# Kernel optimization log

Measured on AMD Instinct MI355X. Metric: run time of the kernel, lower is better.

Reference implementation:

```python
import jax, jax.numpy as jnp
import numpy as np

B, T, I, F, M, O = 256, 512, 128, 512, 512, 128


def setup_inputs() -> dict:
    key = jax.random.key(0)
    ks = jax.random.split(key, 12)
    def lin(k, out_d, in_d):
        std = 1.0 / np.sqrt(in_d)
        kw, kb = jax.random.split(k)
        W = jax.random.uniform(kw, (out_d, in_d), jnp.float32, -std, std)
        b = jax.random.uniform(kb, (out_d,), jnp.float32, -std, std)
        return W, b
    Wi2f, bi2f = lin(ks[0], F, I)
    Wm2f, bm2f = lin(ks[1], F, M)
    Wf2m, bf2m = lin(ks[2], M, F)
    Wm2m, bm2m = lin(ks[3], M, M)
    Wout, bout = lin(ks[4], O, M)
    x = jax.random.normal(ks[5], (B, T, I), jnp.float32)
    m0 = jnp.zeros((B, M), jnp.float32)
    return {"x": x, "m0": m0,
            "Wi2f": Wi2f, "bi2f": bi2f, "Wm2f": Wm2f, "bm2f": bm2f,
            "Wf2m": Wf2m, "bf2m": bf2m, "Wm2m": Wm2m, "bm2m": bm2m,
            "Wout": Wout, "bout": bout}


def reference(x, m0, Wi2f, bi2f, Wm2f, bm2f, Wf2m, bf2m, Wm2m, bm2m, Wout, bout):
    # Precompute input->functional projection for all timesteps (batched GEMM).
    xp = jnp.einsum('bti,fi->btf', x, Wi2f) + bi2f  # (B, T, F)

    def step(m, xp_t):
        f = jnp.tanh(xp_t + m @ Wm2f.T + bm2f)           # (B, F)
        m_new = (f @ Wf2m.T + bf2m) + (m @ Wm2m.T + bm2m)  # (B, M)
        return m_new, m_new

    m_last, _ms = jax.lax.scan(step, m0, jnp.swapaxes(xp, 0, 1))  # ms: (T, B, M)
    # OUTPUT_TYPE.LAST_OUT: output layer applied to final memory state.
    return m_last @ Wout.T + bout  # (B, O)
```

## Files before the change

### kernel.cpp

```cpp
#include <hip/hip_runtime.h>
#include <hip/hip_bf16.h>

typedef __bf16 bf16x8 __attribute__((ext_vector_type(8)));
typedef __bf16 bf16x4 __attribute__((ext_vector_type(4)));
typedef float  f32x4  __attribute__((ext_vector_type(4)));
typedef unsigned int u32;
typedef unsigned long long u64;

static __device__ __forceinline__ void mfma_z(f32x4& d, bf16x8 a, const f32x4& b) {
    asm("v_mfma_f32_16x16x32_bf16 %0, %1, %2, 0"
        : "=&v"(d) : "v"(a), "a"(b));
}
static __device__ __forceinline__ void mfma_a(f32x4& d, bf16x8 a, const f32x4& b) {
    asm("v_mfma_f32_16x16x32_bf16 %0, %1, %2, %0"
        : "+v"(d) : "v"(a), "a"(b));
}
#define ACC_GUARD(e, o) asm volatile("s_nop 7\n\ts_nop 7" : "+v"(e), "+v"(o))

static __device__ __forceinline__ f32x4 mfma16(bf16x8 a, bf16x8 b, f32x4 c) {
    return __builtin_amdgcn_mfma_f32_16x16x32_bf16(a, b, c, 0, 0, 0);
}

static __device__ __forceinline__ void poll_flags(const u32* flags, u32 tgt,
                                                  int lane, u32& alive) {
    if (!alive) return;
    for (u32 it = 0; it < (1u << 20); ++it) {
        u32 v = __hip_atomic_load(&flags[lane & 7], __ATOMIC_RELAXED, __HIP_MEMORY_SCOPE_AGENT);
        if (__all((int)(v >= tgt))) return;
        __builtin_amdgcn_s_sleep(1);
    }
    alive = 0;
}

#define TLEN 512
#define IDIM 128
#define FDIM 512
#define MDIM 512
#define ODIM 128
#define BC   16
#define NGRP 16
#define NCU  8
#define PSTR 520
#define XSTR 136

#define WS_WI   0
#define WS_W2F  (WS_WI  + FDIM*IDIM*2)
#define WS_W2M  (WS_W2F + FDIM*MDIM*2)
#define WS_WF2  (WS_W2M + MDIM*MDIM*2)
#define WS_WO   (WS_WF2 + MDIM*FDIM*2)
#define WS_C    (WS_WO  + ODIM*MDIM*2)
#define WS_D    (WS_C   + FDIM*FDIM*2)
#define WS_B1   (WS_D   + MDIM*FDIM*2)
#define WS_B23  (WS_B1  + FDIM*4)
#define WS_CB   (WS_B23 + MDIM*4)
#define WS_CU   (WS_CB  + FDIM*4)
#define WS_FLG  (WS_CU  + MDIM*4)
#define WS_BUF  (WS_FLG + NGRP*64*4)

#define N_WI  (FDIM*IDIM)
#define N_W2F (FDIM*MDIM)
#define N_W2M (MDIM*MDIM)
#define N_WF2 (MDIM*FDIM)
#define N_WO  (ODIM*MDIM)

__global__ __launch_bounds__(256) void lmn_prep1(
    const float* __restrict__ Wi2f, const float* __restrict__ Wm2f,
    const float* __restrict__ Wm2m, const float* __restrict__ Wf2m,
    const float* __restrict__ Wout,
    const float* __restrict__ bi2f, const float* __restrict__ bm2f,
    const float* __restrict__ bf2m, const float* __restrict__ bm2m,
    __bf16* __restrict__ WI, __bf16* __restrict__ W2F, __bf16* __restrict__ W2M,
    __bf16* __restrict__ WF2, __bf16* __restrict__ WO,
    float* __restrict__ b1, float* __restrict__ b23, u32* __restrict__ flags)
{
    int i = blockIdx.x * 256 + threadIdx.x;
    if (i < N_WI)  { WI[i]  = (__bf16)Wi2f[i]; return; }  i -= N_WI;
    if (i < N_W2F) { W2F[i] = (__bf16)Wm2f[i]; return; }  i -= N_W2F;
    if (i < N_W2M) { W2M[i] = (__bf16)Wm2m[i]; return; }  i -= N_W2M;
    if (i < N_WF2) { WF2[i] = (__bf16)Wf2m[i]; return; }  i -= N_WF2;
    if (i < N_WO)  { WO[i]  = (__bf16)Wout[i]; return; }  i -= N_WO;
    if (i < FDIM)  { b1[i]  = bi2f[i] + bm2f[i]; return; } i -= FDIM;
    if (i < MDIM)  { b23[i] = bf2m[i] + bm2m[i]; return; } i -= MDIM;
    if (i < NGRP * 64) { flags[i] = 0u; return; }
}

__global__ __launch_bounds__(256) void lmn_prep2(
    const float* __restrict__ Wm2f, const float* __restrict__ Wm2m,
    const float* __restrict__ Wf2m,
    const float* __restrict__ b1, const float* __restrict__ b23,
    __bf16* __restrict__ C, __bf16* __restrict__ D,
    float* __restrict__ cb, float* __restrict__ cu)
{
    int bb = blockIdx.x;
    if (bb < 2048) {
        int row = bb >> 1;
        int k   = (bb & 1) * 256 + threadIdx.x;
        const float* A = (row < 512) ? Wm2f : Wm2m;
        int r = row & 511;
        float acc = 0.f;
        for (int j = 0; j < 512; ++j)
            acc += A[(size_t)r * 512 + j] * Wf2m[(size_t)j * 512 + k];
        if (row < 512) C[(size_t)r * 512 + k] = (__bf16)acc;
        else           D[(size_t)r * 512 + k] = (__bf16)acc;
        return;
    }
    int idx = (bb - 2048) * 256 + threadIdx.x;
    if (idx < 512) {
        float acc = b1[idx];
        for (int j = 0; j < 512; ++j) acc += Wm2f[(size_t)idx * 512 + j] * b23[j];
        cb[idx] = acc;
    } else {
        int r = idx - 512;
        float acc = 0.f;
        for (int j = 0; j < 512; ++j) acc += Wm2m[(size_t)r * 512 + j] * b23[j];
        cu[r] = acc;
    }
}

__global__ __launch_bounds__(512, 2) void lmn_scan(
    const float* __restrict__ x, const float* __restrict__ m0,
    const __bf16* __restrict__ WI, const __bf16* __restrict__ W2F,
    const __bf16* __restrict__ W2M, const __bf16* __restrict__ Cm,
    const __bf16* __restrict__ Dm, const __bf16* __restrict__ WF2,
    const __bf16* __restrict__ WO,
    const float* __restrict__ b1, const float* __restrict__ cb,
    const float* __restrict__ cu, const float* __restrict__ b23,
    const float* __restrict__ bout,
    u32* __restrict__ flags_all, __bf16* __restrict__ buf,
    float* __restrict__ out)
{
    __shared__ __bf16 ulds[BC][PSTR];
    __shared__ __bf16 flds[BC][PSTR];
    __shared__ __bf16 xlds[BC][XSTR];

    const int tid  = threadIdx.x;
    const int lane = tid & 63;
    const int w    = tid >> 6;
    const int wq   = w & 3;
    const int l15  = lane & 15;
    const int l4   = lane >> 4;
    const int koff = 8 * l4;
    const bool sRole = (w < 4);

    const int b = blockIdx.x;
    const int g = b & 15;
    const int p = b >> 4;
    const int row0 = g * BC;

    u32* flags = flags_all + g * 64;
    u32  alive = 1;

    const int c0 = 64 * p + 16 * wq + l15;

    f32x4 wgt[36];
    {
        const __bf16* rA = (sRole ? W2F : W2M) + (size_t)c0 * MDIM;
        const __bf16* rC = (sRole ? Cm  : Dm ) + (size_t)c0 * FDIM;
        #pragma unroll
        for (int j = 0; j < 16; ++j) {
            wgt[j]      = *(const f32x4*)&rA[j * 32 + koff];
            wgt[16 + j] = *(const f32x4*)&rC[j * 32 + koff];
        }
        if (sRole) {
            const __bf16* rX = WI + (size_t)c0 * IDIM;
            #pragma unroll
            for (int j = 0; j < 4; ++j) wgt[32 + j] = *(const f32x4*)&rX[j * 32 + koff];
        } else {
            #pragma unroll
            for (int j = 32; j < 36; ++j) wgt[j] = f32x4{0, 0, 0, 0};
        }
        #pragma unroll
        for (int j = 0; j < 36; ++j) asm volatile("" : "+a"(wgt[j]));
    }
    const float b1r = sRole ? b1[c0] : 0.f;
    const float cbr = sRole ? cb[c0] : 0.f;
    const float cur = sRole ? 0.f    : cu[c0];

    #pragma unroll
    for (int i = 0; i < 2; ++i) {
        int c = tid + 512 * i;
        int row = c >> 6, col8 = (c & 63) << 3;
        const float* ms = &m0[(size_t)(row0 + row) * MDIM + col8];
        float4 v0 = ((const float4*)ms)[0], v1 = ((const float4*)ms)[1];
        *(bf16x8*)&ulds[row][col8] =
            bf16x8{(__bf16)v0.x, (__bf16)v0.y, (__bf16)v0.z, (__bf16)v0.w,
                   (__bf16)v1.x, (__bf16)v1.y, (__bf16)v1.z, (__bf16)v1.w};
    }
    if (tid < 256) {
        int rr = tid >> 4, c8 = (tid & 15) << 3;
        const float* xs = &x[(size_t)(row0 + rr) * TLEN * IDIM + c8];
        float4 v0 = ((const float4*)xs)[0], v1 = ((const float4*)xs)[1];
        *(bf16x8*)&xlds[rr][c8] =
            bf16x8{(__bf16)v0.x, (__bf16)v0.y, (__bf16)v0.z, (__bf16)v0.w,
                   (__bf16)v1.x, (__bf16)v1.y, (__bf16)v1.z, (__bf16)v1.w};
    }
    __syncthreads();

    f32x4 accE, accO;
    {
        bf16x8 a0 = *(const bf16x8*)&ulds[l15][0 * 32 + koff];
        bf16x8 a1 = *(const bf16x8*)&ulds[l15][1 * 32 + koff];
        mfma_z(accE, a0, wgt[0]);  mfma_z(accO, a1, wgt[1]);
        #pragma unroll
        for (int j = 2; j < 16; ++j) {
            bf16x8 am = *(const bf16x8*)&ulds[l15][j * 32 + koff];
            if (j & 1) mfma_a(accO, am, wgt[j]);
            else       mfma_a(accE, am, wgt[j]);
        }
        if (sRole) {
            #pragma unroll
            for (int j = 0; j < 4; ++j) {
                bf16x8 ax = *(const bf16x8*)&xlds[l15][j * 32 + koff];
                if (j & 1) mfma_a(accO, ax, wgt[32 + j]);
                else       mfma_a(accE, ax, wgt[32 + j]);
            }
        }
    }

    for (int t = 0; t < TLEN; ++t) {
        __syncthreads();

        ACC_GUARD(accE, accO);
        f32x4 va = accE + accO;
        if (sRole) {
            const float addc = (t == 0) ? b1r : cbr;
            #pragma unroll
            for (int r = 0; r < 4; ++r)
                flds[4 * l4 + r][c0] = (__bf16)tanhf(va[r] + addc);
        } else {
            const float addu = (t == 0) ? 0.f : cur;
            #pragma unroll
            for (int r = 0; r < 4; ++r)
                ulds[4 * l4 + r][c0] = (__bf16)(va[r] + addu);
        }
        __syncthreads();

        const size_t bufbase = (size_t)((t & 1) * NGRP + g) * (2 * BC * MDIM);
        {
            int mat = tid >> 8;
            int rr = (tid & 255) >> 4, c4 = (tid & 15) << 2;
            const __bf16* src = mat ? &flds[rr][64 * p + c4] : &ulds[rr][64 * p + c4];
            u64 v = *(const u64*)src;
            __hip_atomic_store((u64*)(buf + bufbase + (size_t)mat * (BC * MDIM)
                                      + rr * MDIM + 64 * p + c4),
                               v, __ATOMIC_RELAXED, __HIP_MEMORY_SCOPE_AGENT);
        }
        asm volatile("s_waitcnt vmcnt(0)" ::: "memory");
        __syncthreads();
        if (tid == 0)
            __hip_atomic_store(&flags[p], (u32)t + 1u,
                               __ATOMIC_RELAXED, __HIP_MEMORY_SCOPE_AGENT);

        if (tid < 256 && t + 1 < TLEN) {
            int rr = tid >> 4, c8 = (tid & 15) << 3;
            const float* xs = &x[((size_t)(row0 + rr) * TLEN + (t + 1)) * IDIM + c8];
            float4 v0 = ((const float4*)xs)[0], v1 = ((const float4*)xs)[1];
            *(bf16x8*)&xlds[rr][c8] =
                bf16x8{(__bf16)v0.x, (__bf16)v0.y, (__bf16)v0.z, (__bf16)v0.w,
                       (__bf16)v1.x, (__bf16)v1.y, (__bf16)v1.z, (__bf16)v1.w};
        }
        poll_flags(flags, (u32)t + 1u, lane, alive);

        #pragma unroll
        for (int i = 0; i < 4; ++i) {
            int c = tid + 512 * i;
            int mat = c >> 10, rem = c & 1023;
            int row = rem >> 6, col8 = (rem & 63) << 3;
            const __bf16* src = buf + bufbase + (size_t)mat * (BC * MDIM)
                              + row * MDIM + col8;
            u64 lo = __hip_atomic_load((const u64*)src,     __ATOMIC_RELAXED, __HIP_MEMORY_SCOPE_AGENT);
            u64 hi = __hip_atomic_load((const u64*)src + 1, __ATOMIC_RELAXED, __HIP_MEMORY_SCOPE_AGENT);
            union { u64 q[2]; bf16x8 v; } uu; uu.q[0] = lo; uu.q[1] = hi;
            if (mat) *(bf16x8*)&flds[row][col8] = uu.v;
            else     *(bf16x8*)&ulds[row][col8] = uu.v;
        }
        __syncthreads();

        if (t == TLEN - 1) break;

        {
            bf16x8 a0 = *(const bf16x8*)&ulds[l15][0 * 32 + koff];
            bf16x8 a1 = *(const bf16x8*)&ulds[l15][1 * 32 + koff];
            mfma_z(accE, a0, wgt[0]);  mfma_z(accO, a1, wgt[1]);
            #pragma unroll
            for (int j = 2; j < 16; ++j) {
                bf16x8 am = *(const bf16x8*)&ulds[l15][j * 32 + koff];
                if (j & 1) mfma_a(accO, am, wgt[j]);
                else       mfma_a(accE, am, wgt[j]);
            }
            #pragma unroll
            for (int j = 0; j < 16; ++j) {
                bf16x8 af = *(const bf16x8*)&flds[l15][j * 32 + koff];
                if (j & 1) mfma_a(accO, af, wgt[16 + j]);
                else       mfma_a(accE, af, wgt[16 + j]);
            }
            if (sRole) {
                #pragma unroll
                for (int j = 0; j < 4; ++j) {
                    bf16x8 ax = *(const bf16x8*)&xlds[l15][j * 32 + koff];
                    if (j & 1) mfma_a(accO, ax, wgt[32 + j]);
                    else       mfma_a(accE, ax, wgt[32 + j]);
                }
            }
        }
    }

    if (p == 0) {
        f32x4 ma[4];
        #pragma unroll
        for (int nt = 0; nt < 4; ++nt) {
            int ct = 64 * w + 16 * nt + l15;
            f32x4 acc = {0, 0, 0, 0};
            #pragma unroll
            for (int j = 0; j < 16; ++j) {
                bf16x8 af = *(const bf16x8*)&flds[l15][j * 32 + koff];
                bf16x8 bw = *(const bf16x8*)&WF2[(size_t)ct * FDIM + j * 32 + koff];
                acc = mfma16(af, bw, acc);
            }
            ma[nt] = acc;
        }
        #pragma unroll
        for (int nt = 0; nt < 4; ++nt) {
            int ct = 64 * w + 16 * nt + l15;
            #pragma unroll
            for (int r = 0; r < 4; ++r) {
                float mv = ma[nt][r] + (float)ulds[4 * l4 + r][ct] + b23[ct];
                ulds[4 * l4 + r][ct] = (__bf16)mv;
            }
        }
        __syncthreads();
        const int oc = 16 * w + l15;
        const __bf16* ro = WO + (size_t)oc * MDIM;
        f32x4 oe = {0, 0, 0, 0}, oo = {0, 0, 0, 0};
        #pragma unroll
        for (int j = 0; j < 16; ++j) {
            bf16x8 am = *(const bf16x8*)&ulds[l15][j * 32 + koff];
            bf16x8 bw = *(const bf16x8*)&ro[j * 32 + koff];
            if (j & 1) oo = mfma16(am, bw, oo); else oe = mfma16(am, bw, oe);
        }
        f32x4 oa = oe + oo;
        const float bo = bout[oc];
        #pragma unroll
        for (int r = 0; r < 4; ++r)
            out[(size_t)(row0 + 4 * l4 + r) * ODIM + oc] = oa[r] + bo;
    }
}

extern "C" void kernel_launch(void* const* d_in, const int* in_sizes, int n_in,
                              void* d_out, int out_size, void* d_ws, size_t ws_size,
                              hipStream_t stream)
{
    const float* x    = (const float*)d_in[0];
    const float* m0   = (const float*)d_in[1];
    const float* Wi2f = (const float*)d_in[2];
    const float* bi2f = (const float*)d_in[3];
    const float* Wm2f = (const float*)d_in[4];
    const float* bm2f = (const float*)d_in[5];
    const float* Wf2m = (const float*)d_in[6];
    const float* bf2m = (const float*)d_in[7];
    const float* Wm2m = (const float*)d_in[8];
    const float* bm2m = (const float*)d_in[9];
    const float* Wout = (const float*)d_in[10];
    const float* bout = (const float*)d_in[11];

    char* ws = (char*)d_ws;
    __bf16* WI  = (__bf16*)(ws + WS_WI);
    __bf16* W2F = (__bf16*)(ws + WS_W2F);
    __bf16* W2M = (__bf16*)(ws + WS_W2M);
    __bf16* WF2 = (__bf16*)(ws + WS_WF2);
    __bf16* WO  = (__bf16*)(ws + WS_WO);
    __bf16* Cm  = (__bf16*)(ws + WS_C);
    __bf16* Dm  = (__bf16*)(ws + WS_D);
    float*  b1  = (float*)(ws + WS_B1);
    float*  b23 = (float*)(ws + WS_B23);
    float*  cb  = (float*)(ws + WS_CB);
    float*  cu  = (float*)(ws + WS_CU);
    u32*    flg = (u32*)(ws + WS_FLG);
    __bf16* buf = (__bf16*)(ws + WS_BUF);

    const int prep1_total = N_WI + N_W2F + N_W2M + N_WF2 + N_WO
                          + FDIM + MDIM + NGRP * 64;
    lmn_prep1<<<(prep1_total + 255) / 256, 256, 0, stream>>>(
        Wi2f, Wm2f, Wm2m, Wf2m, Wout, bi2f, bm2f, bf2m, bm2m,
        WI, W2F, W2M, WF2, WO, b1, b23, flg);

    lmn_prep2<<<2052, 256, 0, stream>>>(Wm2f, Wm2m, Wf2m, b1, b23, Cm, Dm, cb, cu);

    lmn_scan<<<NGRP * NCU, 512, 0, stream>>>(
        x, m0, WI, W2F, W2M, Cm, Dm, WF2, WO,
        b1, cb, cu, b23, bout, flg, buf, (float*)d_out);
}
```

Baseline: 1.881 ms.

## Split each batch group into two half-groups to overlap exchange with compute

Splits each 16-row batch chunk into two independent 8-row sub-batches with their own LDS buffers, global exchange buffers and flags. The timestep loop now alternates between the two, so one sub-batch's cross-block exchange and polling can overlap with the other's MFMA work. The cost is that each MFMA now uses only 8 of its 16 rows, so matrix work per row doubles, and there are more barriers and flag round-trips per step.

```diff
diff --git a/kernel.cpp b/kernel.cpp
--- a/kernel.cpp
+++ b/kernel.cpp
@@ -38,10 +38,12 @@
 #define MDIM 512
 #define ODIM 128
 #define BC   16
+#define BCS  8
 #define NGRP 16
 #define NCU  8
 #define PSTR 520
 #define XSTR 136
+#define BUFBLK (2*BCS*MDIM)
 
 #define WS_WI   0
 #define WS_W2F  (WS_WI  + FDIM*IDIM*2)
@@ -129,9 +131,10 @@
     u32* __restrict__ flags_all, __bf16* __restrict__ buf,
     float* __restrict__ out)
 {
-    __shared__ __bf16 ulds[BC][PSTR];
-    __shared__ __bf16 flds[BC][PSTR];
-    __shared__ __bf16 xlds[BC][XSTR];
+    __shared__ __bf16 ulds[2][BCS][PSTR];
+    __shared__ __bf16 flds[2][BCS][PSTR];
+    __shared__ __bf16 xlds[2][BCS][XSTR];
+    __shared__ __bf16 sstg[2][2][BCS][72];
 
     const int tid  = threadIdx.x;
     const int lane = tid & 63;
@@ -140,6 +143,7 @@
     const int l15  = lane & 15;
     const int l4   = lane >> 4;
     const int koff = 8 * l4;
+    const int ar   = l15 & 7;
     const bool sRole = (w < 4);
 
     const int b = blockIdx.x;
@@ -147,7 +151,8 @@
     const int p = b >> 4;
     const int row0 = g * BC;
 
-    u32* flags = flags_all + g * 64;
+    u32* flagS0 = flags_all + g * 64 + 16;
+    u32* flagS1 = flags_all + g * 64 + 24;
     u32  alive = 1;
 
     const int c0 = 64 * p + 16 * wq + l15;
@@ -177,172 +182,212 @@
     const float cur = sRole ? 0.f    : cu[c0];
 
     #pragma unroll
-    for (int i = 0; i < 2; ++i) {
-        int c = tid + 512 * i;
-        int row = c >> 6, col8 = (c & 63) << 3;
-        const float* ms = &m0[(size_t)(row0 + row) * MDIM + col8];
-        float4 v0 = ((const float4*)ms)[0], v1 = ((const float4*)ms)[1];
-        *(bf16x8*)&ulds[row][col8] =
-            bf16x8{(__bf16)v0.x, (__bf16)v0.y, (__bf16)v0.z, (__bf16)v0.w,
-                   (__bf16)v1.x, (__bf16)v1.y, (__bf16)v1.z, (__bf16)v1.w};
-    }
-    if (tid < 256) {
-        int rr = tid >> 4, c8 = (tid & 15) << 3;
-        const float* xs = &x[(size_t)(row0 + rr) * TLEN * IDIM + c8];
-        float4 v0 = ((const float4*)xs)[0], v1 = ((const float4*)xs)[1];
-        *(bf16x8*)&xlds[rr][c8] =
-            bf16x8{(__bf16)v0.x, (__bf16)v0.y, (__bf16)v0.z, (__bf16)v0.w,
-                   (__bf16)v1.x, (__bf16)v1.y, (__bf16)v1.z, (__bf16)v1.w};
-    }
-    __syncthreads();
-
-    f32x4 accE, accO;
-    {
-        bf16x8 a0 = *(const bf16x8*)&ulds[l15][0 * 32 + koff];
-        bf16x8 a1 = *(const bf16x8*)&ulds[l15][1 * 32 + koff];
-        mfma_z(accE, a0, wgt[0]);  mfma_z(accO, a1, wgt[1]);
-        #pragma unroll
-        for (int j = 2; j < 16; ++j) {
-            bf16x8 am = *(const bf16x8*)&ulds[l15][j * 32 + koff];
-            if (j & 1) mfma_a(accO, am, wgt[j]);
-            else       mfma_a(accE, am, wgt[j]);
-        }
-        if (sRole) {
-            #pragma unroll
-            for (int j = 0; j < 4; ++j) {
-                bf16x8 ax = *(const bf16x8*)&xlds[l15][j * 32 + koff];
-                if (j & 1) mfma_a(accO, ax, wgt[32 + j]);
-                else       mfma_a(accE, ax, wgt[32 + j]);
-            }
-        }
-    }
-
-    for (int t = 0; t < TLEN; ++t) {
+    for (int s = 0; s < 2; ++s) {
+        {
+            int row = tid >> 6, col8 = (tid & 63) << 3;
+            const float* ms = &m0[(size_t)(row0 + 8 * s + row) * MDIM + col8];
+            float4 v0 = ((const float4*)ms)[0], v1 = ((const float4*)ms)[1];
+            *(bf16x8*)&ulds[s][row][col8] =
+                bf16x8{(__bf16)v0.x, (__bf16)v0.y, (__bf16)v0.z, (__bf16)v0.w,
+                       (__bf16)v1.x, (__bf16)v1.y, (__bf16)v1.z, (__bf16)v1.w};
+        }
+        if (tid < 128) {
+            int rr = tid >> 4, c8 = (tid & 15) << 3;
+            const float* xs = &x[(size_t)(row0 + 8 * s + rr) * TLEN * IDIM + c8];
+            float4 v0 = ((const float4*)xs)[0], v1 = ((const float4*)xs)[1];
+            *(bf16x8*)&xlds[s][rr][c8] =
+                bf16x8{(__bf16)v0.x, (__bf16)v0.y, (__bf16)v0.z, (__bf16)v0.w,
+                       (__bf16)v1.x, (__bf16)v1.y, (__bf16)v1.z, (__bf16)v1.w};
+        }
         __syncthreads();
-
+        f32x4 accE, accO;
+        {
+            bf16x8 a0 = *(const bf16x8*)&ulds[s][ar][0 * 32 + koff];
+            bf16x8 a1 = *(const bf16x8*)&ulds[s][ar][1 * 32 + koff];
+            mfma_z(accE, a0, wgt[0]);  mfma_z(accO, a1, wgt[1]);
+            #pragma unroll
+            for (int j = 2; j < 16; ++j) {
+                bf16x8 am = *(const bf16x8*)&ulds[s][ar][j * 32 + koff];
+                if (j & 1) mfma_a(accO, am, wgt[j]);
+                else       mfma_a(accE, am, wgt[j]);
+            }
+            if (sRole) {
+                #pragma unroll
+                for (int j = 0; j < 4; ++j) {
+                    bf16x8 ax = *(const bf16x8*)&xlds[s][ar][j * 32 + koff];
+                    if (j & 1) mfma_a(accO, ax, wgt[32 + j]);
+                    else       mfma_a(accE, ax, wgt[32 + j]);
+                }
+            }
+        }
         ACC_GUARD(accE, accO);
         f32x4 va = accE + accO;
-        if (sRole) {
-            const float addc = (t == 0) ? b1r : cbr;
-            #pragma unroll
-            for (int r = 0; r < 4; ++r)
-                flds[4 * l4 + r][c0] = (__bf16)tanhf(va[r] + addc);
-        } else {
-            const float addu = (t == 0) ? 0.f : cur;
-            #pragma unroll
-            for (int r = 0; r < 4; ++r)
-                ulds[4 * l4 + r][c0] = (__bf16)(va[r] + addu);
+        {
+            int mat = sRole ? 1 : 0;
+            #pragma unroll
+            for (int r = 0; r < 4; ++r) {
+                int rr = 4 * l4 + r;
+                if (rr < 8)
+                    sstg[s][mat][rr][16 * wq + l15] =
+                        sRole ? (__bf16)tanhf(va[r] + b1r) : (__bf16)va[r];
+            }
         }
         __syncthreads();
-
-        const size_t bufbase = (size_t)((t & 1) * NGRP + g) * (2 * BC * MDIM);
-        {
-            int mat = tid >> 8;
-            int rr = (tid & 255) >> 4, c4 = (tid & 15) << 2;
-            const __bf16* src = mat ? &flds[rr][64 * p + c4] : &ulds[rr][64 * p + c4];
-            u64 v = *(const u64*)src;
-            __hip_atomic_store((u64*)(buf + bufbase + (size_t)mat * (BC * MDIM)
-                                      + rr * MDIM + 64 * p + c4),
-                               v, __ATOMIC_RELAXED, __HIP_MEMORY_SCOPE_AGENT);
+        if (tid < 256) {
+            int mat = tid >> 7, idx = tid & 127;
+            int rr = idx >> 4, c4 = (idx & 15) << 2;
+            u64 v = *(const u64*)&sstg[s][mat][rr][c4];
+            __bf16* dst = buf + ((size_t)(0 * NGRP + g) * 2 + s) * BUFBLK
+                        + (size_t)mat * (BCS * MDIM) + rr * MDIM + 64 * p + c4;
+            __hip_atomic_store((u64*)dst, v, __ATOMIC_RELAXED, __HIP_MEMORY_SCOPE_AGENT);
+        }
+        if (tid < 128) {
+            int rr = tid >> 4, c8 = (tid & 15) << 3;
+            const float* xs = &x[((size_t)(row0 + 8 * s + rr) * TLEN + 1) * IDIM + c8];
+            float4 v0 = ((const float4*)xs)[0], v1 = ((const float4*)xs)[1];
+            *(bf16x8*)&xlds[s][rr][c8] =
+                bf16x8{(__bf16)v0.x, (__bf16)v0.y, (__bf16)v0.z, (__bf16)v0.w,
+                       (__bf16)v1.x, (__bf16)v1.y, (__bf16)v1.z, (__bf16)v1.w};
         }
         asm volatile("s_waitcnt vmcnt(0)" ::: "memory");
         __syncthreads();
         if (tid == 0)
-            __hip_atomic_store(&flags[p], (u32)t + 1u,
+            __hip_atomic_store((s ? flagS1 : flagS0) + p, 1u,
                                __ATOMIC_RELAXED, __HIP_MEMORY_SCOPE_AGENT);
-
-        if (tid < 256 && t + 1 < TLEN) {
-            int rr = tid >> 4, c8 = (tid & 15) << 3;
-            const float* xs = &x[((size_t)(row0 + rr) * TLEN + (t + 1)) * IDIM + c8];
-            float4 v0 = ((const float4*)xs)[0], v1 = ((const float4*)xs)[1];
-            *(bf16x8*)&xlds[rr][c8] =
-                bf16x8{(__bf16)v0.x, (__bf16)v0.y, (__bf16)v0.z, (__bf16)v0.w,
-                       (__bf16)v1.x, (__bf16)v1.y, (__bf16)v1.z, (__bf16)v1.w};
-        }
-        poll_flags(flags, (u32)t + 1u, lane, alive);
-
+    }
+
+    for (int t = 0; t < TLEN; ++t) {
+        const int gpar = t & 1, epar = (t + 1) & 1;
         #pragma unroll
-        for (int i = 0; i < 4; ++i) {
-            int c = tid + 512 * i;
-            int mat = c >> 10, rem = c & 1023;
-            int row = rem >> 6, col8 = (rem & 63) << 3;
-            const __bf16* src = buf + bufbase + (size_t)mat * (BC * MDIM)
-                              + row * MDIM + col8;
-            u64 lo = __hip_atomic_load((const u64*)src,     __ATOMIC_RELAXED, __HIP_MEMORY_SCOPE_AGENT);
-            u64 hi = __hip_atomic_load((const u64*)src + 1, __ATOMIC_RELAXED, __HIP_MEMORY_SCOPE_AGENT);
-            union { u64 q[2]; bf16x8 v; } uu; uu.q[0] = lo; uu.q[1] = hi;
-            if (mat) *(bf16x8*)&flds[row][col8] = uu.v;
-            else     *(bf16x8*)&ulds[row][col8] = uu.v;
-        }
-        __syncthreads();
-
-        if (t == TLEN - 1) break;
-
-        {
-            bf16x8 a0 = *(const bf16x8*)&ulds[l15][0 * 32 + koff];
-            bf16x8 a1 = *(const bf16x8*)&ulds[l15][1 * 32 + koff];
-            mfma_z(accE, a0, wgt[0]);  mfma_z(accO, a1, wgt[1]);
-            #pragma unroll
-            for (int j = 2; j < 16; ++j) {
-                bf16x8 am = *(const bf16x8*)&ulds[l15][j * 32 + koff];
-                if (j & 1) mfma_a(accO, am, wgt[j]);
-                else       mfma_a(accE, am, wgt[j]);
-            }
+        for (int s = 0; s < 2; ++s) {
+            u32* flg = s ? flagS1 : flagS0;
+            poll_flags(flg, (u32)t + 1u, lane, alive);
+            const __bf16* gbase = buf + ((size_t)(gpar * NGRP + g) * 2 + s) * BUFBLK;
+            #pragma unroll
+            for (int i = 0; i < 2; ++i) {
+                int c = tid + 512 * i;
+                int mat = c >> 9, rem = c & 511;
+                int row = rem >> 6, col8 = (rem & 63) << 3;
+                const __bf16* src = gbase + (size_t)mat * (BCS * MDIM) + row * MDIM + col8;
+                u64 lo = __hip_atomic_load((const u64*)src,     __ATOMIC_RELAXED, __HIP_MEMORY_SCOPE_AGENT);
+                u64 hi = __hip_atomic_load((const u64*)src + 1, __ATOMIC_RELAXED, __HIP_MEMORY_SCOPE_AGENT);
+                union { u64 q[2]; bf16x8 v; } uu; uu.q[0] = lo; uu.q[1] = hi;
+                if (mat) *(bf16x8*)&flds[s][row][col8] = uu.v;
+                else     *(bf16x8*)&ulds[s][row][col8] = uu.v;
+            }
+            __syncthreads();
+            if (t < TLEN - 1) {
+                f32x4 accE, accO;
+                bf16x8 a0 = *(const bf16x8*)&ulds[s][ar][0 * 32 + koff];
+                bf16x8 a1 = *(const bf16x8*)&ulds[s][ar][1 * 32 + koff];
+                mfma_z(accE, a0, wgt[0]);  mfma_z(accO, a1, wgt[1]);
+                #pragma unroll
+                for (int j = 2; j < 16; ++j) {
+                    bf16x8 am = *(const bf16x8*)&ulds[s][ar][j * 32 + koff];
+                    if (j & 1) mfma_a(accO, am, wgt[j]);
+                    else       mfma_a(accE, am, wgt[j]);
+                }
+                #pragma unroll
+                for (int j = 0; j < 16; ++j) {
+                    bf16x8 af = *(const bf16x8*)&flds[s][ar][j * 32 + koff];
+                    if (j & 1) mfma_a(accO, af, wgt[16 + j]);
+                    else       mfma_a(accE, af, wgt[16 + j]);
+                }
+                if (sRole) {
+                    #pragma unroll
+                    for (int j = 0; j < 4; ++j) {
+                        bf16x8 ax = *(const bf16x8*)&xlds[s][ar][j * 32 + koff];
+                        if (j & 1) mfma_a(accO, ax, wgt[32 + j]);
+                        else       mfma_a(accE, ax, wgt[32 + j]);
+                    }
+                }
+                ACC_GUARD(accE, accO);
+                f32x4 va = accE + accO;
+                int mat = sRole ? 1 : 0;
+                #pragma unroll
+                for (int r = 0; r < 4; ++r) {
+                    int rr = 4 * l4 + r;
+                    if (rr < 8)
+                        sstg[s][mat][rr][16 * wq + l15] =
+                            sRole ? (__bf16)tanhf(va[r] + cbr) : (__bf16)(va[r] + cur);
+                }
+            }
+            __syncthreads();
+            if (t < TLEN - 1) {
+                if (tid < 256) {
+                    int mat = tid >> 7, idx = tid & 127;
+                    int rr = idx >> 4, c4 = (idx & 15) << 2;
+                    u64 v = *(const u64*)&sstg[s][mat][rr][c4];
+                    __bf16* dst = buf + ((size_t)(epar * NGRP + g) * 2 + s) * BUFBLK
+                                + (size_t)mat * (BCS * MDIM) + rr * MDIM + 64 * p + c4;
+                    __hip_atomic_store((u64*)dst, v, __ATOMIC_RELAXED, __HIP_MEMORY_SCOPE_AGENT);
+                }
+                if (tid < 128 && t + 2 < TLEN) {
+                    int rr = tid >> 4, c8 = (tid & 15) << 3;
+                    const float* xs = &x[((size_t)(row0 + 8 * s + rr) * TLEN + (t + 2)) * IDIM + c8];
+                    float4 v0 = ((const float4*)xs)[0], v1 = ((const float4*)xs)[1];
+                    *(bf16x8*)&xlds[s][rr][c8] =
+                        bf16x8{(__bf16)v0.x, (__bf16)v0.y, (__bf16)v0.z, (__bf16)v0.w,
+                               (__bf16)v1.x, (__bf16)v1.y, (__bf16)v1.z, (__bf16)v1.w};
+                }
+            }
+            asm volatile("s_waitcnt vmcnt(0)" ::: "memory");
+            __syncthreads();
+            if (t < TLEN - 1 && tid == 0)
+                __hip_atomic_store(flg + p, (u32)t + 2u,
+                                   __ATOMIC_RELAXED, __HIP_MEMORY_SCOPE_AGENT);
+        }
+    }
+
+    __syncthreads();
+    if (p == 0) {
+        #pragma unroll
+        for (int s = 0; s < 2; ++s) {
+            f32x4 ma[4];
+            #pragma unroll
+            for (int nt = 0; nt < 4; ++nt) {
+                int ct = 64 * w + 16 * nt + l15;
+                f32x4 acc = {0, 0, 0, 0};
+                #pragma unroll
+                for (int j = 0; j < 16; ++j) {
+                    bf16x8 af = *(const bf16x8*)&flds[s][ar][j * 32 + koff];
+                    bf16x8 bw = *(const bf16x8*)&WF2[(size_t)ct * FDIM + j * 32 + koff];
+                    acc = mfma16(af, bw, acc);
+                }
+                ma[nt] = acc;
+            }
+            #pragma unroll
+            for (int nt = 0; nt < 4; ++nt) {
+                int ct = 64 * w + 16 * nt + l15;
+                #pragma unroll
+                for (int r = 0; r < 4; ++r) {
+                    int rr = 4 * l4 + r;
+                    if (rr < 8) {
+                        float mv = ma[nt][r] + (float)ulds[s][rr][ct] + b23[ct];
+                        ulds[s][rr][ct] = (__bf16)mv;
+                    }
+                }
+            }
+            __syncthreads();
+            const int oc = 16 * w + l15;
+            const __bf16* ro = WO + (size_t)oc * MDIM;
+            f32x4 oe = {0, 0, 0, 0}, oo = {0, 0, 0, 0};
             #pragma unroll
             for (int j = 0; j < 16; ++j) {
-                bf16x8 af = *(const bf16x8*)&flds[l15][j * 32 + koff];
-                if (j & 1) mfma_a(accO, af, wgt[16 + j]);
-                else       mfma_a(accE, af, wgt[16 + j]);
-            }
-            if (sRole) {
-                #pragma unroll
-                for (int j = 0; j < 4; ++j) {
-                    bf16x8 ax = *(const bf16x8*)&xlds[l15][j * 32 + koff];
-                    if (j & 1) mfma_a(accO, ax, wgt[32 + j]);
-                    else       mfma_a(accE, ax, wgt[32 + j]);
-                }
-            }
-        }
-    }
-
-    if (p == 0) {
-        f32x4 ma[4];
-        #pragma unroll
-        for (int nt = 0; nt < 4; ++nt) {
-            int ct = 64 * w + 16 * nt + l15;
-            f32x4 acc = {0, 0, 0, 0};
-            #pragma unroll
-            for (int j = 0; j < 16; ++j) {
-                bf16x8 af = *(const bf16x8*)&flds[l15][j * 32 + koff];
-                bf16x8 bw = *(const bf16x8*)&WF2[(size_t)ct * FDIM + j * 32 + koff];
-                acc = mfma16(af, bw, acc);
-            }
-            ma[nt] = acc;
-        }
-        #pragma unroll
-        for (int nt = 0; nt < 4; ++nt) {
-            int ct = 64 * w + 16 * nt + l15;
+                bf16x8 am = *(const bf16x8*)&ulds[s][ar][j * 32 + koff];
+                bf16x8 bw = *(const bf16x8*)&ro[j * 32 + koff];
+                if (j & 1) oo = mfma16(am, bw, oo); else oe = mfma16(am, bw, oe);
+            }
+            f32x4 oa = oe + oo;
+            const float bo = bout[oc];
             #pragma unroll
             for (int r = 0; r < 4; ++r) {
-                float mv = ma[nt][r] + (float)ulds[4 * l4 + r][ct] + b23[ct];
-                ulds[4 * l4 + r][ct] = (__bf16)mv;
-            }
-        }
-        __syncthreads();
-        const int oc = 16 * w + l15;
-        const __bf16* ro = WO + (size_t)oc * MDIM;
-        f32x4 oe = {0, 0, 0, 0}, oo = {0, 0, 0, 0};
-        #pragma unroll
-        for (int j = 0; j < 16; ++j) {
-            bf16x8 am = *(const bf16x8*)&ulds[l15][j * 32 + koff];
-            bf16x8 bw = *(const bf16x8*)&ro[j * 32 + koff];
-            if (j & 1) oo = mfma16(am, bw, oo); else oe = mfma16(am, bw, oe);
-        }
-        f32x4 oa = oe + oo;
-        const float bo = bout[oc];
-        #pragma unroll
-        for (int r = 0; r < 4; ++r)
-            out[(size_t)(row0 + 4 * l4 + r) * ODIM + oc] = oa[r] + bo;
+                int rr = 4 * l4 + r;
+                if (rr < 8)
+                    out[(size_t)(row0 + 8 * s + rr) * ODIM + oc] = oa[r] + bo;
+            }
+            __syncthreads();
+        }
     }
 }
 
```

Result: slower. 3.290 ms (+74.9%).
